# Optimization experiments

Measured on AMD Instinct MI355X. Metric: run time of the kernel, lower is better.

Reference implementation:

```python
import jax, jax.numpy as jnp
import numpy as np

DIM = 1024
HID = 2816
N_ROUTED = 7  # num_experts - num_shared_experts
TOPK = 2
B, S = 4, 2048


def _expert(x, wg, wu, wd):
    # DeepSeekExpertLayer: down(silu(gate(x)) * up(x)); weights stored [in, out]
    return (jax.nn.silu(x @ wg) * (x @ wu)) @ wd


def setup_inputs() -> dict:
    key = jax.random.key(0)
    ks = jax.random.split(key, 9)
    s = 0.02
    x = jax.random.normal(ks[0], (B, S, DIM), jnp.float32)
    shared_gate = jax.random.normal(ks[1], (DIM, HID), jnp.float32) * s
    shared_up = jax.random.normal(ks[2], (DIM, HID), jnp.float32) * s
    shared_down = jax.random.normal(ks[3], (HID, DIM), jnp.float32) * s
    routed_gate = jax.random.normal(ks[4], (N_ROUTED, DIM, HID), jnp.float32) * s
    routed_up = jax.random.normal(ks[5], (N_ROUTED, DIM, HID), jnp.float32) * s
    routed_down = jax.random.normal(ks[6], (N_ROUTED, HID, DIM), jnp.float32) * s
    Wr = jax.random.normal(ks[7], (DIM, N_ROUTED), jnp.float32) * s
    # NOTE: original inits routing_bias to zeros (degenerate routing since logits
    # are MULTIPLIED by it); use random values so routing is non-trivial.
    routing_bias = jax.random.normal(ks[8], (N_ROUTED,), jnp.float32)
    return dict(x=x, shared_gate=shared_gate, shared_up=shared_up, shared_down=shared_down,
                routed_gate=routed_gate, routed_up=routed_up, routed_down=routed_down,
                Wr=Wr, routing_bias=routing_bias)


def reference(x, shared_gate, shared_up, shared_down,
              routed_gate, routed_up, routed_down, Wr, routing_bias):
    b, s, d = x.shape
    n_exp = routed_gate.shape[0]
    # shared expert path (num_shared_experts == 1, no division)
    shared_out = _expert(x, shared_gate, shared_up, shared_down)
    # router: note logits are MULTIPLIED by routing_bias (faithful to source)
    logits = (x @ Wr) * routing_bias            # [b, s, E]
    probs = jax.nn.sigmoid(logits)
    scores, idx = jax.lax.top_k(probs, TOPK)    # [b, s, k]
    scores = scores / scores.sum(-1, keepdims=True)
    # per-token per-expert combine weight via scatter-add of top-k scores
    t = b * s
    xf = x.reshape(t, d)
    weights = jnp.zeros((t, n_exp), x.dtype).at[
        jnp.arange(t)[:, None], idx.reshape(t, TOPK)].add(scores.reshape(t, TOPK))
    combined = jnp.zeros_like(xf)
    for e in range(n_exp):  # static small loop over experts
        combined = combined + _expert(xf, routed_gate[e], routed_up[e], routed_down[e]) * weights[:, e:e + 1]
    return shared_out + combined.reshape(b, s, d)
```

## Files before the change

### kernel.cpp

```cpp
#include <hip/hip_runtime.h>
#include <hip/hip_bf16.h>

#define DIM 1024
#define HID 2816
#define NEXP 7
#define TOKENS 8192

#define MW2_XB    0ull
#define MW2_WGU   16777216ull
#define MW2_WD    109051904ull
#define MW2_H     155189248ull
#define MW2_TOK   298647552ull
#define MW2_WGT   298749440ull
#define MW2_SLT   298851328ull
#define MW2_META  298916864ull
#define MW2_NEED  298918912ull

#define MW_XB    0ull
#define MW_H     16777216ull
#define MW_WGU   114098176ull
#define MW_WD    206372864ull
#define MW_TOK   252510208ull
#define MW_WGT   252579328ull
#define MW_META  252648448ull
#define MW_NEED  252650496ull

typedef __bf16 bf16x8 __attribute__((ext_vector_type(8)));
typedef float f32x4 __attribute__((ext_vector_type(4)));

static __device__ __forceinline__ unsigned short f2b(float f) {
  union { float f; unsigned int i; } c; c.f = f;
  unsigned int i = c.i;
  unsigned int r = (i + 0x7fffu + ((i >> 16) & 1u)) >> 16;
  return (unsigned short)r;
}

static __device__ __forceinline__ void gload16(const void* g, void* l) {
  __builtin_amdgcn_global_load_lds(
      (const __attribute__((address_space(1))) unsigned int*)g,
      (__attribute__((address_space(3))) unsigned int*)l, 16, 0, 0);
}

__global__ __launch_bounds__(256, 2) void router_kernel(
    const float* __restrict__ X,
    const float* __restrict__ Wr,
    const float* __restrict__ bias,
    int* __restrict__ eidx,
    float* __restrict__ ew)
{
  __shared__ float wr[DIM * NEXP];
  for (int i = threadIdx.x; i < DIM * NEXP; i += 256) wr[i] = Wr[i];
  __syncthreads();
  int t = blockIdx.x * 256 + threadIdx.x;
  float acc[NEXP];
#pragma unroll
  for (int e = 0; e < NEXP; ++e) acc[e] = 0.f;
  const float* xp = X + (size_t)t * DIM;
  for (int d0 = 0; d0 < DIM; d0 += 4) {
    float4 xv = *(const float4*)(xp + d0);
    const float* xs = (const float*)&xv;
#pragma unroll
    for (int j = 0; j < 4; ++j) {
      float xf = xs[j];
#pragma unroll
      for (int e = 0; e < NEXP; ++e) acc[e] += xf * wr[(d0 + j) * NEXP + e];
    }
  }
  float p[NEXP];
#pragma unroll
  for (int e = 0; e < NEXP; ++e)
    p[e] = 1.f / (1.f + __expf(-acc[e] * bias[e]));
  float best = -1.f; int bi = 0;
#pragma unroll
  for (int e = 0; e < NEXP; ++e) if (p[e] > best) { best = p[e]; bi = e; }
  float sec = -1.f; int si = 0;
#pragma unroll
  for (int e = 0; e < NEXP; ++e) if (e != bi && p[e] > sec) { sec = p[e]; si = e; }
  float s = best + sec;
  eidx[t] = bi | (si << 8);
  ((float2*)ew)[t] = make_float2(best / s, sec / s);
}

__global__ __launch_bounds__(256) void xcvt_kernel(
    const float* __restrict__ X, unsigned short* __restrict__ Xb)
{
  int i = (blockIdx.x * 256 + threadIdx.x) * 8;
  float4 v0 = *(const float4*)&X[i];
  float4 v1 = *(const float4*)&X[i + 4];
  unsigned short o[8];
  o[0] = f2b(v0.x); o[1] = f2b(v0.y); o[2] = f2b(v0.z); o[3] = f2b(v0.w);
  o[4] = f2b(v1.x); o[5] = f2b(v1.y); o[6] = f2b(v1.z); o[7] = f2b(v1.w);
  *(int4*)&Xb[i] = *(const int4*)o;
}

__global__ __launch_bounds__(256) void build2_kernel(
    const int* __restrict__ eidx, const float* __restrict__ ew,
    int* __restrict__ tok, float* __restrict__ wgt,
    int2* __restrict__ slt, int* __restrict__ meta)
{
  __shared__ int cnt[NEXP], fill[NEXP], ofs[NEXP];
  const int tid = threadIdx.x;
  const int lane = tid & 63, wid = tid >> 6;
  if (tid < NEXP) { cnt[tid] = 0; fill[tid] = 0; }
  for (int i = tid; i < TOKENS; i += 256) { tok[i] = i; wgt[i] = 1.f; }
  __syncthreads();
  const unsigned long long lmask = (1ull << lane) - 1ull;
  for (int base = wid * 64; base < TOKENS; base += 256) {
    int t = base + lane;
    int p = eidx[t];
    int e0 = p & 0xff, e1 = (p >> 8) & 0xff;
#pragma unroll
    for (int e = 0; e < NEXP; ++e) {
      unsigned long long m0 = __ballot(e0 == e);
      unsigned long long m1 = __ballot(e1 == e);
      if (lane == 0) {
        int tot = __popcll(m0) + __popcll(m1);
        if (tot) atomicAdd(&cnt[e], tot);
      }
    }
  }
  __syncthreads();
  if (tid == 0) {
    int o = 0, nb = 0;
    meta[0] = TOKENS; meta[8] = 0;
    for (int i = 0; i < TOKENS / 128; ++i) meta[17 + nb++] = 0 | (i << 4);
    for (int e = 0; e < NEXP; ++e) {
      ofs[e] = o;
      meta[1 + e] = cnt[e];
      meta[9 + e] = TOKENS + o;
      int b = (cnt[e] + 127) >> 7;
      for (int i = 0; i < b; ++i) meta[17 + nb++] = (e + 1) | (i << 4);
      o += b << 7;
    }
    meta[16] = nb;
  }
  __syncthreads();
  for (int base = wid * 64; base < TOKENS; base += 256) {
    int t = base + lane;
    int p = eidx[t];
    int e0 = p & 0xff, e1 = (p >> 8) & 0xff;
    float2 w = ((const float2*)ew)[t];
    int s0 = 0, s1 = 0;
#pragma unroll
    for (int e = 0; e < NEXP; ++e) {
      unsigned long long m0 = __ballot(e0 == e);
      unsigned long long m1 = __ballot(e1 == e);
      int tot = __popcll(m0) + __popcll(m1);
      int wb = 0;
      if (lane == 0 && tot) wb = atomicAdd(&fill[e], tot);
      wb = __shfl(wb, 0);
      if (e0 == e) {
        int sl = TOKENS + ofs[e] + wb + __popcll(m0 & lmask);
        tok[sl] = t; wgt[sl] = w.x; s0 = sl;
      }
      if (e1 == e) {
        int sl = TOKENS + ofs[e] + wb + __popcll(m0) + __popcll(m1 & lmask);
        tok[sl] = t; wgt[sl] = w.y; s1 = sl;
      }
    }
    slt[t] = make_int2(s0, s1);
  }
}

__global__ __launch_bounds__(256) void transpose_all_kernel(
    const float* __restrict__ sg, const float* __restrict__ su, const float* __restrict__ sd,
    const float* __restrict__ rg, const float* __restrict__ ru, const float* __restrict__ rd,
    unsigned short* __restrict__ WguA, unsigned short* __restrict__ WdA)
{
  int b = blockIdx.x;
  int e = b / 2112, r = b % 2112;
  int m = r / 704, q2 = r % 704;
  const float* src; unsigned short* dst; int K, N, nb, kb;
  if (m == 0) {
    src = e ? rg + (size_t)(e - 1) * DIM * HID : sg;
    dst = WguA + (size_t)e * (2 * (size_t)HID * DIM);
    K = DIM; N = HID; nb = q2 % 44; kb = q2 / 44;
  } else if (m == 1) {
    src = e ? ru + (size_t)(e - 1) * DIM * HID : su;
    dst = WguA + (size_t)e * (2 * (size_t)HID * DIM) + (size_t)HID * DIM;
    K = DIM; N = HID; nb = q2 % 44; kb = q2 / 44;
  } else {
    src = e ? rd + (size_t)(e - 1) * HID * DIM : sd;
    dst = WdA + (size_t)e * ((size_t)HID * DIM);
    K = HID; N = DIM; nb = q2 % 16; kb = q2 / 16;
  }
  __shared__ unsigned short t[64][72];
  const int n0 = nb * 64, k0 = kb * 64;
  const int tid = threadIdx.x;
  const int kl = tid >> 4, nl = (tid & 15) * 4;
#pragma unroll
  for (int i = 0; i < 4; ++i) {
    int k = kl + i * 16;
    float4 v = *(const float4*)&src[(size_t)(k0 + k) * N + n0 + nl];
    t[nl + 0][k] = f2b(v.x); t[nl + 1][k] = f2b(v.y);
    t[nl + 2][k] = f2b(v.z); t[nl + 3][k] = f2b(v.w);
  }
  __syncthreads();
  const int nl2 = tid >> 3, kc = (tid & 7) * 8;
#pragma unroll
  for (int i = 0; i < 2; ++i) {
    int n = nl2 + i * 32;
    *(int4*)&dst[(size_t)(n0 + n) * K + k0 + kc] = *(const int4*)&t[n][kc];
  }
}


__global__ __launch_bounds__(256, 2) void gateup_all_kernel(
    const unsigned short* __restrict__ Xb,
    const unsigned short* __restrict__ WguA,
    const int* __restrict__ tok, const float* __restrict__ wgt,
    const int* __restrict__ meta,
    unsigned short* __restrict__ H)
{
  const int yb = blockIdx.y;
  if (yb >= meta[16]) return;
  const int ent = meta[17 + yb];
  const int e = ent & 15, mb = ent >> 4;
  const int cnt = meta[e];
  const int pofs = meta[8 + e];
  const unsigned short* Wg = WguA + (size_t)e * (2 * (size_t)HID * DIM);
  const unsigned short* Wu = Wg + (size_t)HID * DIM;

  __shared__ __align__(16) unsigned short As[128 * 64];
  __shared__ __align__(16) unsigned short Bgs[64 * 64];
  __shared__ __align__(16) unsigned short Bus[64 * 64];
  __shared__ float wl[128];

  const int n0 = blockIdx.x * 64;
  const int tid = threadIdx.x;
  const int lane = tid & 63;
  const int w = tid >> 6;
  const int wm = (w & 1) * 64;
  const int wn = (w >> 1) * 32;
  const int c = lane & 15;
  const int q = lane >> 4;
  const int cx = c & 7;

  if (tid < 128)
    wl[tid] = (mb * 128 + tid < cnt) ? wgt[pofs + mb * 128 + tid] : 0.f;

  const int r8 = lane >> 3;
  const int swz = ((lane & 7) ^ r8) * 8;
  const int wrow = w * 8 + r8;

  const unsigned short* aptr[4];
#pragma unroll
  for (int i = 0; i < 4; ++i) {
    int s = mb * 128 + i * 32 + wrow;
    int t = (s < cnt) ? tok[pofs + s] : 0;
    aptr[i] = Xb + (size_t)t * DIM + swz;
  }
  const unsigned short* gptr[2];
  const unsigned short* uptr[2];
#pragma unroll
  for (int i = 0; i < 2; ++i) {
    gptr[i] = Wg + (size_t)(n0 + i * 32 + wrow) * DIM + swz;
    uptr[i] = Wu + (size_t)(n0 + i * 32 + wrow) * DIM + swz;
  }

  f32x4 accg[4][2], accu[4][2];
#pragma unroll
  for (int mi = 0; mi < 4; ++mi)
#pragma unroll
    for (int ni = 0; ni < 2; ++ni) {
      accg[mi][ni] = {0.f, 0.f, 0.f, 0.f};
      accu[mi][ni] = {0.f, 0.f, 0.f, 0.f};
    }

  for (int k0 = 0; k0 < DIM; k0 += 64) {
    __syncthreads();
#pragma unroll
    for (int i = 0; i < 4; ++i) gload16(aptr[i] + k0, &As[i * 2048 + tid * 8]);
#pragma unroll
    for (int i = 0; i < 2; ++i) {
      gload16(gptr[i] + k0, &Bgs[i * 2048 + tid * 8]);
      gload16(uptr[i] + k0, &Bus[i * 2048 + tid * 8]);
    }
    __syncthreads();
#pragma unroll
    for (int h = 0; h < 2; ++h) {
      const int go = ((h * 4 + q) ^ cx) * 8;
      bf16x8 a[4], bg[2], bu[2];
#pragma unroll
      for (int mi = 0; mi < 4; ++mi)
        a[mi] = *(const bf16x8*)&As[(wm + mi * 16 + c) * 64 + go];
#pragma unroll
      for (int ni = 0; ni < 2; ++ni) {
        bg[ni] = *(const bf16x8*)&Bgs[(wn + ni * 16 + c) * 64 + go];
        bu[ni] = *(const bf16x8*)&Bus[(wn + ni * 16 + c) * 64 + go];
      }
#pragma unroll
      for (int mi = 0; mi < 4; ++mi)
#pragma unroll
        for (int ni = 0; ni < 2; ++ni) {
          accg[mi][ni] = __builtin_amdgcn_mfma_f32_16x16x32_bf16(a[mi], bg[ni], accg[mi][ni], 0, 0, 0);
          accu[mi][ni] = __builtin_amdgcn_mfma_f32_16x16x32_bf16(a[mi], bu[ni], accu[mi][ni], 0, 0, 0);
        }
    }
  }
#pragma unroll
  for (int mi = 0; mi < 4; ++mi)
#pragma unroll
    for (int ni = 0; ni < 2; ++ni)
#pragma unroll
      for (int r = 0; r < 4; ++r) {
        int row = wm + mi * 16 + q * 4 + r;
        int col = wn + ni * 16 + c;
        float g = accg[mi][ni][r];
        float u = accu[mi][ni][r];
        float h = (g / (1.f + __expf(-g))) * u * wl[row];
        H[(size_t)(pofs + mb * 128 + row) * HID + n0 + col] = f2b(h);
      }
}

__global__ __launch_bounds__(256, 2) void down_all_kernel(
    const unsigned short* __restrict__ Hm,
    const unsigned short* __restrict__ WdA,
    const int* __restrict__ meta,
    float* __restrict__ P)
{
  const int yb = blockIdx.y;
  if (yb >= meta[16]) return;
  const int ent = meta[17 + yb];
  const int e = ent & 15, mb = ent >> 4;
  const int pofs = meta[8 + e];
  const unsigned short* WdT = WdA + (size_t)e * ((size_t)HID * DIM);

  __shared__ __align__(16) unsigned short As[128 * 64];
  __shared__ __align__(16) unsigned short Bs[128 * 64];
  const int n0 = blockIdx.x * 128;
  const int tid = threadIdx.x;
  const int lane = tid & 63;
  const int w4 = tid >> 6;
  const int wm = (w4 & 1) * 64;
  const int wn = (w4 >> 1) * 64;
  const int c = lane & 15;
  const int q = lane >> 4;
  const int cx = c & 7;

  const int r8 = lane >> 3;
  const int swz = ((lane & 7) ^ r8) * 8;
  const int wrow = w4 * 8 + r8;

  const unsigned short* aptr[4];
  const unsigned short* bptr[4];
#pragma unroll
  for (int i = 0; i < 4; ++i) {
    aptr[i] = Hm + (size_t)(pofs + mb * 128 + i * 32 + wrow) * HID + swz;
    bptr[i] = WdT + (size_t)(n0 + i * 32 + wrow) * HID + swz;
  }

  f32x4 acc[4][4];
#pragma unroll
  for (int mi = 0; mi < 4; ++mi)
#pragma unroll
    for (int ni = 0; ni < 4; ++ni) acc[mi][ni] = {0.f, 0.f, 0.f, 0.f};

  for (int k0 = 0; k0 < HID; k0 += 64) {
    __syncthreads();
#pragma unroll
    for (int i = 0; i < 4; ++i) {
      gload16(aptr[i] + k0, &As[i * 2048 + tid * 8]);
      gload16(bptr[i] + k0, &Bs[i * 2048 + tid * 8]);
    }
    __syncthreads();
#pragma unroll
    for (int h = 0; h < 2; ++h) {
      const int go = ((h * 4 + q) ^ cx) * 8;
      bf16x8 a[4], b[4];
#pragma unroll
      for (int mi = 0; mi < 4; ++mi)
        a[mi] = *(const bf16x8*)&As[(wm + mi * 16 + c) * 64 + go];
#pragma unroll
      for (int ni = 0; ni < 4; ++ni)
        b[ni] = *(const bf16x8*)&Bs[(wn + ni * 16 + c) * 64 + go];
#pragma unroll
      for (int mi = 0; mi < 4; ++mi)
#pragma unroll
        for (int ni = 0; ni < 4; ++ni)
          acc[mi][ni] = __builtin_amdgcn_mfma_f32_16x16x32_bf16(a[mi], b[ni], acc[mi][ni], 0, 0, 0);
    }
  }
#pragma unroll
  for (int mi = 0; mi < 4; ++mi)
#pragma unroll
    for (int r = 0; r < 4; ++r) {
      int prow = pofs + mb * 128 + wm + mi * 16 + q * 4 + r;
#pragma unroll
      for (int ni = 0; ni < 4; ++ni) {
        int col = n0 + wn + ni * 16 + c;
        P[(size_t)prow * DIM + col] = acc[mi][ni][r];
      }
    }
}

__global__ __launch_bounds__(256) void combine_kernel(
    const float* __restrict__ P, const int2* __restrict__ slt,
    float* __restrict__ out)
{
  const int t = blockIdx.x;
  const int2 s = slt[t];
  const int d = threadIdx.x;
  float4 a = ((const float4*)(P + (size_t)t * DIM))[d];
  float4 b = ((const float4*)(P + (size_t)s.x * DIM))[d];
  float4 cc = ((const float4*)(P + (size_t)s.y * DIM))[d];
  float4 o;
  o.x = a.x + b.x + cc.x; o.y = a.y + b.y + cc.y;
  o.z = a.z + b.z + cc.z; o.w = a.w + b.w + cc.w;
  ((float4*)(out + (size_t)t * DIM))[d] = o;
}

__global__ __launch_bounds__(256) void build_kernel(
    const int* __restrict__ eidx, const float* __restrict__ ew,
    int* __restrict__ tok, float* __restrict__ wgt, int* __restrict__ meta,
    int padmode)
{
  __shared__ int cnt[NEXP], fill[NEXP], ofs[NEXP];
  if (threadIdx.x < NEXP) { cnt[threadIdx.x] = 0; fill[threadIdx.x] = 0; }
  __syncthreads();
  for (int t = threadIdx.x; t < TOKENS; t += 256) {
    int p = eidx[t];
    atomicAdd(&cnt[p & 0xff], 1);
    atomicAdd(&cnt[(p >> 8) & 0xff], 1);
  }
  __syncthreads();
  if (threadIdx.x == 0) {
    int o = 0, nb = 0;
    for (int e = 0; e < NEXP; ++e) {
      ofs[e] = o;
      meta[e] = cnt[e];
      meta[8 + e] = o;
      if (padmode) {
        int b = (cnt[e] + 127) >> 7;
        for (int i = 0; i < b; ++i) meta[16 + nb++] = e | (i << 3);
        o += b << 7;
      } else {
        o += cnt[e];
      }
    }
    meta[15] = nb;
  }
  __syncthreads();
  for (int t = threadIdx.x; t < TOKENS; t += 256) {
    int p = eidx[t];
    int e0 = p & 0xff, e1 = (p >> 8) & 0xff;
    float2 w = ((const float2*)ew)[t];
    int p0 = ofs[e0] + atomicAdd(&fill[e0], 1);
    tok[p0] = t; wgt[p0] = w.x;
    int p1 = ofs[e1] + atomicAdd(&fill[e1], 1);
    tok[p1] = t; wgt[p1] = w.y;
  }
}

__global__ __launch_bounds__(256, 2) void gateup_kernel(
    const unsigned short* __restrict__ Xb,
    const unsigned short* __restrict__ Wgu,
    unsigned short* __restrict__ H)
{
  __shared__ __align__(16) unsigned short As[128 * 64];
  __shared__ __align__(16) unsigned short Bgs[64 * 64];
  __shared__ __align__(16) unsigned short Bus[64 * 64];
  const int m0 = blockIdx.y * 128;
  const int n0 = blockIdx.x * 64;
  const int tid = threadIdx.x;
  const int lane = tid & 63;
  const int w = tid >> 6;
  const int wm = (w & 1) * 64;
  const int wn = (w >> 1) * 32;
  const int c = lane & 15;
  const int q = lane >> 4;
  const int cx = c & 7;
  const unsigned short* Wg = Wgu;
  const unsigned short* Wu = Wgu + (size_t)HID * DIM;
  const int r8 = lane >> 3;
  const int swz = ((lane & 7) ^ r8) * 8;
  const int wrow = w * 8 + r8;
  const unsigned short* aptr[4];
#pragma unroll
  for (int i = 0; i < 4; ++i)
    aptr[i] = Xb + (size_t)(m0 + i * 32 + wrow) * DIM + swz;
  const unsigned short* gptr[2];
  const unsigned short* uptr[2];
#pragma unroll
  for (int i = 0; i < 2; ++i) {
    gptr[i] = Wg + (size_t)(n0 + i * 32 + wrow) * DIM + swz;
    uptr[i] = Wu + (size_t)(n0 + i * 32 + wrow) * DIM + swz;
  }
  f32x4 accg[4][2], accu[4][2];
#pragma unroll
  for (int mi = 0; mi < 4; ++mi)
#pragma unroll
    for (int ni = 0; ni < 2; ++ni) {
      accg[mi][ni] = {0.f, 0.f, 0.f, 0.f};
      accu[mi][ni] = {0.f, 0.f, 0.f, 0.f};
    }
  for (int k0 = 0; k0 < DIM; k0 += 64) {
    __syncthreads();
#pragma unroll
    for (int i = 0; i < 4; ++i) gload16(aptr[i] + k0, &As[i * 2048 + tid * 8]);
#pragma unroll
    for (int i = 0; i < 2; ++i) {
      gload16(gptr[i] + k0, &Bgs[i * 2048 + tid * 8]);
      gload16(uptr[i] + k0, &Bus[i * 2048 + tid * 8]);
    }
    __syncthreads();
#pragma unroll
    for (int h = 0; h < 2; ++h) {
      const int go = ((h * 4 + q) ^ cx) * 8;
      bf16x8 a[4], bg[2], bu[2];
#pragma unroll
      for (int mi = 0; mi < 4; ++mi)
        a[mi] = *(const bf16x8*)&As[(wm + mi * 16 + c) * 64 + go];
#pragma unroll
      for (int ni = 0; ni < 2; ++ni) {
        bg[ni] = *(const bf16x8*)&Bgs[(wn + ni * 16 + c) * 64 + go];
        bu[ni] = *(const bf16x8*)&Bus[(wn + ni * 16 + c) * 64 + go];
      }
#pragma unroll
      for (int mi = 0; mi < 4; ++mi)
#pragma unroll
        for (int ni = 0; ni < 2; ++ni) {
          accg[mi][ni] = __builtin_amdgcn_mfma_f32_16x16x32_bf16(a[mi], bg[ni], accg[mi][ni], 0, 0, 0);
          accu[mi][ni] = __builtin_amdgcn_mfma_f32_16x16x32_bf16(a[mi], bu[ni], accu[mi][ni], 0, 0, 0);
        }
    }
  }
#pragma unroll
  for (int mi = 0; mi < 4; ++mi)
#pragma unroll
    for (int ni = 0; ni < 2; ++ni)
#pragma unroll
      for (int r = 0; r < 4; ++r) {
        int row = wm + mi * 16 + q * 4 + r;
        int col = wn + ni * 16 + c;
        float g = accg[mi][ni][r];
        float u = accu[mi][ni][r];
        float h = (g / (1.f + __expf(-g))) * u;
        H[(size_t)(m0 + row) * HID + n0 + col] = f2b(h);
      }
}

__global__ __launch_bounds__(256, 2) void gateup_sparse_all_kernel(
    const unsigned short* __restrict__ Xb,
    const unsigned short* __restrict__ WguR,
    const int* __restrict__ tok, const float* __restrict__ wgt,
    const int* __restrict__ meta,
    unsigned short* __restrict__ H)
{
  const int yb = blockIdx.y;
  if (yb >= meta[15]) return;
  const int bm = meta[16 + yb];
  const int e = bm & 7, mb = bm >> 3;
  const int cnt = meta[e];
  const int pofs = meta[8 + e];
  const unsigned short* Wgu = WguR + (size_t)e * (2 * (size_t)HID * DIM);
  __shared__ __align__(16) unsigned short As[128 * 64];
  __shared__ __align__(16) unsigned short Bgs[64 * 64];
  __shared__ __align__(16) unsigned short Bus[64 * 64];
  __shared__ float wl[128];
  const int n0 = blockIdx.x * 64;
  const int tid = threadIdx.x;
  const int lane = tid & 63;
  const int w = tid >> 6;
  const int wm = (w & 1) * 64;
  const int wn = (w >> 1) * 32;
  const int c = lane & 15;
  const int q = lane >> 4;
  const int cx = c & 7;
  if (tid < 128)
    wl[tid] = (mb * 128 + tid < cnt) ? wgt[pofs + mb * 128 + tid] : 0.f;
  const unsigned short* Wg = Wgu;
  const unsigned short* Wu = Wgu + (size_t)HID * DIM;
  const int r8 = lane >> 3;
  const int swz = ((lane & 7) ^ r8) * 8;
  const int wrow = w * 8 + r8;
  const unsigned short* aptr[4];
#pragma unroll
  for (int i = 0; i < 4; ++i) {
    int s = mb * 128 + i * 32 + wrow;
    int t = (s < cnt) ? tok[pofs + s] : 0;
    aptr[i] = Xb + (size_t)t * DIM + swz;
  }
  const unsigned short* gptr[2];
  const unsigned short* uptr[2];
#pragma unroll
  for (int i = 0; i < 2; ++i) {
    gptr[i] = Wg + (size_t)(n0 + i * 32 + wrow) * DIM + swz;
    uptr[i] = Wu + (size_t)(n0 + i * 32 + wrow) * DIM + swz;
  }
  f32x4 accg[4][2], accu[4][2];
#pragma unroll
  for (int mi = 0; mi < 4; ++mi)
#pragma unroll
    for (int ni = 0; ni < 2; ++ni) {
      accg[mi][ni] = {0.f, 0.f, 0.f, 0.f};
      accu[mi][ni] = {0.f, 0.f, 0.f, 0.f};
    }
  for (int k0 = 0; k0 < DIM; k0 += 64) {
    __syncthreads();
#pragma unroll
    for (int i = 0; i < 4; ++i) gload16(aptr[i] + k0, &As[i * 2048 + tid * 8]);
#pragma unroll
    for (int i = 0; i < 2; ++i) {
      gload16(gptr[i] + k0, &Bgs[i * 2048 + tid * 8]);
      gload16(uptr[i] + k0, &Bus[i * 2048 + tid * 8]);
    }
    __syncthreads();
#pragma unroll
    for (int h = 0; h < 2; ++h) {
      const int go = ((h * 4 + q) ^ cx) * 8;
      bf16x8 a[4], bg[2], bu[2];
#pragma unroll
      for (int mi = 0; mi < 4; ++mi)
        a[mi] = *(const bf16x8*)&As[(wm + mi * 16 + c) * 64 + go];
#pragma unroll
      for (int ni = 0; ni < 2; ++ni) {
        bg[ni] = *(const bf16x8*)&Bgs[(wn + ni * 16 + c) * 64 + go];
        bu[ni] = *(const bf16x8*)&Bus[(wn + ni * 16 + c) * 64 + go];
      }
#pragma unroll
      for (int mi = 0; mi < 4; ++mi)
#pragma unroll
        for (int ni = 0; ni < 2; ++ni) {
          accg[mi][ni] = __builtin_amdgcn_mfma_f32_16x16x32_bf16(a[mi], bg[ni], accg[mi][ni], 0, 0, 0);
          accu[mi][ni] = __builtin_amdgcn_mfma_f32_16x16x32_bf16(a[mi], bu[ni], accu[mi][ni], 0, 0, 0);
        }
    }
  }
#pragma unroll
  for (int mi = 0; mi < 4; ++mi)
#pragma unroll
    for (int ni = 0; ni < 2; ++ni)
#pragma unroll
      for (int r = 0; r < 4; ++r) {
        int row = wm + mi * 16 + q * 4 + r;
        int col = wn + ni * 16 + c;
        float g = accg[mi][ni][r];
        float u = accu[mi][ni][r];
        float h = (g / (1.f + __expf(-g))) * u * wl[row];
        H[(size_t)(pofs + mb * 128 + row) * HID + n0 + col] = f2b(h);
      }
}

__global__ __launch_bounds__(256, 2) void down_dense_kernel(
    const unsigned short* __restrict__ Hm,
    const unsigned short* __restrict__ WdT,
    float* __restrict__ out)
{
  __shared__ __align__(16) unsigned short As[128 * 64];
  __shared__ __align__(16) unsigned short Bs[128 * 64];
  const int m0 = blockIdx.y * 128;
  const int n0 = blockIdx.x * 128;
  const int tid = threadIdx.x;
  const int lane = tid & 63;
  const int w4 = tid >> 6;
  const int wm = (w4 & 1) * 64;
  const int wn = (w4 >> 1) * 64;
  const int c = lane & 15;
  const int q = lane >> 4;
  const int cx = c & 7;
  const int r8 = lane >> 3;
  const int swz = ((lane & 7) ^ r8) * 8;
  const int wrow = w4 * 8 + r8;
  const unsigned short* aptr[4];
  const unsigned short* bptr[4];
#pragma unroll
  for (int i = 0; i < 4; ++i) {
    aptr[i] = Hm + (size_t)(m0 + i * 32 + wrow) * HID + swz;
    bptr[i] = WdT + (size_t)(n0 + i * 32 + wrow) * HID + swz;
  }
  f32x4 acc[4][4];
#pragma unroll
  for (int mi = 0; mi < 4; ++mi)
#pragma unroll
    for (int ni = 0; ni < 4; ++ni) acc[mi][ni] = {0.f, 0.f, 0.f, 0.f};
  for (int k0 = 0; k0 < HID; k0 += 64) {
    __syncthreads();
#pragma unroll
    for (int i = 0; i < 4; ++i) {
      gload16(aptr[i] + k0, &As[i * 2048 + tid * 8]);
      gload16(bptr[i] + k0, &Bs[i * 2048 + tid * 8]);
    }
    __syncthreads();
#pragma unroll
    for (int h = 0; h < 2; ++h) {
      const int go = ((h * 4 + q) ^ cx) * 8;
      bf16x8 a[4], b[4];
#pragma unroll
      for (int mi = 0; mi < 4; ++mi)
        a[mi] = *(const bf16x8*)&As[(wm + mi * 16 + c) * 64 + go];
#pragma unroll
      for (int ni = 0; ni < 4; ++ni)
        b[ni] = *(const bf16x8*)&Bs[(wn + ni * 16 + c) * 64 + go];
#pragma unroll
      for (int mi = 0; mi < 4; ++mi)
#pragma unroll
        for (int ni = 0; ni < 4; ++ni)
          acc[mi][ni] = __builtin_amdgcn_mfma_f32_16x16x32_bf16(a[mi], b[ni], acc[mi][ni], 0, 0, 0);
    }
  }
#pragma unroll
  for (int mi = 0; mi < 4; ++mi)
#pragma unroll
    for (int r = 0; r < 4; ++r) {
      int trow = m0 + wm + mi * 16 + q * 4 + r;
#pragma unroll
      for (int ni = 0; ni < 4; ++ni) {
        int col = n0 + wn + ni * 16 + c;
        out[(size_t)trow * DIM + col] = acc[mi][ni][r];
      }
    }
}

__global__ __launch_bounds__(256, 2) void down_sparse_all_kernel(
    const unsigned short* __restrict__ Hm,
    const unsigned short* __restrict__ WdR,
    const int* __restrict__ tok, const int* __restrict__ meta,
    float* __restrict__ out)
{
  const int yb = blockIdx.y;
  if (yb >= meta[15]) return;
  const int bm = meta[16 + yb];
  const int e = bm & 7, mb = bm >> 3;
  const int cnt = meta[e];
  const int pofs = meta[8 + e];
  const unsigned short* WdT = WdR + (size_t)e * ((size_t)HID * DIM);
  const int kbase = blockIdx.z * (HID / 2);
  __shared__ __align__(16) unsigned short As[128 * 64];
  __shared__ __align__(16) unsigned short Bs[128 * 64];
  __shared__ int tl[128];
  const int n0 = blockIdx.x * 128;
  const int tid = threadIdx.x;
  const int lane = tid & 63;
  const int w4 = tid >> 6;
  const int wm = (w4 & 1) * 64;
  const int wn = (w4 >> 1) * 64;
  const int c = lane & 15;
  const int q = lane >> 4;
  const int cx = c & 7;
  if (tid < 128)
    tl[tid] = (mb * 128 + tid < cnt) ? tok[pofs + mb * 128 + tid] : 0;
  const int r8 = lane >> 3;
  const int swz = ((lane & 7) ^ r8) * 8;
  const int wrow = w4 * 8 + r8;
  const unsigned short* aptr[4];
  const unsigned short* bptr[4];
#pragma unroll
  for (int i = 0; i < 4; ++i) {
    aptr[i] = Hm + (size_t)(pofs + mb * 128 + i * 32 + wrow) * HID + kbase + swz;
    bptr[i] = WdT + (size_t)(n0 + i * 32 + wrow) * HID + kbase + swz;
  }
  f32x4 acc[4][4];
#pragma unroll
  for (int mi = 0; mi < 4; ++mi)
#pragma unroll
    for (int ni = 0; ni < 4; ++ni) acc[mi][ni] = {0.f, 0.f, 0.f, 0.f};
  for (int k0 = 0; k0 < HID / 2; k0 += 64) {
    __syncthreads();
#pragma unroll
    for (int i = 0; i < 4; ++i) {
      gload16(aptr[i] + k0, &As[i * 2048 + tid * 8]);
      gload16(bptr[i] + k0, &Bs[i * 2048 + tid * 8]);
    }
    __syncthreads();
#pragma unroll
    for (int h = 0; h < 2; ++h) {
      const int go = ((h * 4 + q) ^ cx) * 8;
      bf16x8 a[4], b[4];
#pragma unroll
      for (int mi = 0; mi < 4; ++mi)
        a[mi] = *(const bf16x8*)&As[(wm + mi * 16 + c) * 64 + go];
#pragma unroll
      for (int ni = 0; ni < 4; ++ni)
        b[ni] = *(const bf16x8*)&Bs[(wn + ni * 16 + c) * 64 + go];
#pragma unroll
      for (int mi = 0; mi < 4; ++mi)
#pragma unroll
        for (int ni = 0; ni < 4; ++ni)
          acc[mi][ni] = __builtin_amdgcn_mfma_f32_16x16x32_bf16(a[mi], b[ni], acc[mi][ni], 0, 0, 0);
    }
  }
#pragma unroll
  for (int mi = 0; mi < 4; ++mi)
#pragma unroll
    for (int r = 0; r < 4; ++r) {
      int lr = wm + mi * 16 + q * 4 + r;
      if (mb * 128 + lr < cnt) {
        int t = tl[lr];
#pragma unroll
        for (int ni = 0; ni < 4; ++ni) {
          int col = n0 + wn + ni * 16 + c;
          atomicAdd(&out[(size_t)t * DIM + col], acc[mi][ni][r]);
        }
      }
    }
}

extern "C" void kernel_launch(void* const* d_in, const int* in_sizes, int n_in,
                              void* d_out, int out_size, void* d_ws, size_t ws_size,
                              hipStream_t stream) {
  (void)in_sizes; (void)n_in; (void)out_size;
  const float* x   = (const float*)d_in[0];
  const float* sg  = (const float*)d_in[1];
  const float* su  = (const float*)d_in[2];
  const float* sd  = (const float*)d_in[3];
  const float* rg  = (const float*)d_in[4];
  const float* ru  = (const float*)d_in[5];
  const float* rd  = (const float*)d_in[6];
  const float* wrr = (const float*)d_in[7];
  const float* rb  = (const float*)d_in[8];
  float* out = (float*)d_out;

  char* ws = (char*)d_ws;
  dim3 blk(256);

  if (ws_size >= MW2_NEED) {
    unsigned short* Xb   = (unsigned short*)(ws + MW2_XB);
    unsigned short* WguA = (unsigned short*)(ws + MW2_WGU);
    unsigned short* WdA  = (unsigned short*)(ws + MW2_WD);
    unsigned short* H    = (unsigned short*)(ws + MW2_H);
    int*   tok           = (int*)(ws + MW2_TOK);
    float* wgt           = (float*)(ws + MW2_WGT);
    int2*  slt           = (int2*)(ws + MW2_SLT);
    int*   meta          = (int*)(ws + MW2_META);
    float* P             = (float*)ws;
    int*   eidx = (int*)H;
    float* ew   = (float*)((char*)H + 32768);

    router_kernel<<<dim3(TOKENS / 256), blk, 0, stream>>>(x, wrr, rb, eidx, ew);
    xcvt_kernel<<<dim3(TOKENS * DIM / (8 * 256)), blk, 0, stream>>>(x, Xb);
    build2_kernel<<<dim3(1), blk, 0, stream>>>(eidx, ew, tok, wgt, slt, meta);
    transpose_all_kernel<<<dim3(8 * 2112), blk, 0, stream>>>(sg, su, sd, rg, ru, rd, WguA, WdA);
    gateup_all_kernel<<<dim3(HID / 64, 199), blk, 0, stream>>>(Xb, WguA, tok, wgt, meta, H);
    down_all_kernel<<<dim3(DIM / 128, 199), blk, 0, stream>>>(H, WdA, meta, P);
    combine_kernel<<<dim3(TOKENS), blk, 0, stream>>>(P, slt, out);
  } else {
    unsigned short* Xb   = (unsigned short*)(ws + MW_XB);
    unsigned short* H    = (unsigned short*)(ws + MW_H);
    unsigned short* WguA = (unsigned short*)(ws + MW_WGU);
    unsigned short* WdA  = (unsigned short*)(ws + MW_WD);
    int*   tok           = (int*)(ws + MW_TOK);
    float* wgt           = (float*)(ws + MW_WGT);
    int*   meta          = (int*)(ws + MW_META);
    int*   eidx = (int*)H;
    float* ew   = (float*)((char*)H + 32768);

    router_kernel<<<dim3(TOKENS / 256), blk, 0, stream>>>(x, wrr, rb, eidx, ew);
    xcvt_kernel<<<dim3(TOKENS * DIM / (8 * 256)), blk, 0, stream>>>(x, Xb);
    build_kernel<<<dim3(1), blk, 0, stream>>>(eidx, ew, tok, wgt, meta, 1);
    transpose_all_kernel<<<dim3(8 * 2112), blk, 0, stream>>>(sg, su, sd, rg, ru, rd, WguA, WdA);
    gateup_kernel<<<dim3(HID / 64, TOKENS / 128), blk, 0, stream>>>(Xb, WguA, H);
    down_dense_kernel<<<dim3(DIM / 128, TOKENS / 128), blk, 0, stream>>>(H, WdA, out);
    const unsigned short* WguRt = WguA + 2 * (size_t)HID * DIM;
    const unsigned short* WdRt  = WdA + (size_t)HID * DIM;
    gateup_sparse_all_kernel<<<dim3(HID / 64, 135), blk, 0, stream>>>(Xb, WguRt, tok, wgt, meta, H);
    down_sparse_all_kernel<<<dim3(DIM / 128, 135, 2), blk, 0, stream>>>(H, WdRt, tok, meta, out);
  }
}
```

Before: 972.8 us.

## Rewrite grouped gate/up GEMM as 512-thread 256-row tile with triple-buffered pipeline

Replaces the gate/up expert GEMM with a 512-thread kernel that handles 256-token tiles, triple-buffers the A and B operand tiles in shared memory, and interleaves async global loads with MFMA phases. It uses explicit barriers, waitcnt, sched_barrier and setprio to overlap memory with compute. Routing metadata is rebuilt with 256-row padding for gateup and a separate 128-row block list for the down kernel, and the workspace layout grows accordingly. The goal is to hide load latency and improve reuse of the weight tiles. The cost is more padding waste per expert, a large shared-memory footprint that limits occupancy, and hand-written wait counts that must be exactly right for correctness.

```diff
diff --git a/kernel.cpp b/kernel.cpp
--- a/kernel.cpp
+++ b/kernel.cpp
@@ -5,16 +5,17 @@
 #define HID 2816
 #define NEXP 7
 #define TOKENS 8192
-
-#define MW2_XB    0ull
-#define MW2_WGU   16777216ull
-#define MW2_WD    109051904ull
-#define MW2_H     155189248ull
-#define MW2_TOK   298647552ull
-#define MW2_WGT   298749440ull
-#define MW2_SLT   298851328ull
-#define MW2_META  298916864ull
-#define MW2_NEED  298918912ull
+#define NT16 (DIM / 64)
+
+#define MW3_XB    0ull
+#define MW3_WGU   16777216ull
+#define MW3_WD    109051904ull
+#define MW3_H     155189248ull
+#define MW3_TOK   303693824ull
+#define MW3_WGT   303799296ull
+#define MW3_SLT   303904768ull
+#define MW3_META  303970304ull
+#define MW3_NEED  303972352ull
 
 #define MW_XB    0ull
 #define MW_H     16777216ull
@@ -93,7 +94,7 @@
   *(int4*)&Xb[i] = *(const int4*)o;
 }
 
-__global__ __launch_bounds__(256) void build2_kernel(
+__global__ __launch_bounds__(256) void build3_kernel(
     const int* __restrict__ eidx, const float* __restrict__ ew,
     int* __restrict__ tok, float* __restrict__ wgt,
     int2* __restrict__ slt, int* __restrict__ meta)
@@ -121,18 +122,20 @@
   }
   __syncthreads();
   if (tid == 0) {
-    int o = 0, nb = 0;
+    int o = 0, nb = 0, nb2 = 0;
     meta[0] = TOKENS; meta[8] = 0;
-    for (int i = 0; i < TOKENS / 128; ++i) meta[17 + nb++] = 0 | (i << 4);
+    for (int i = 0; i < TOKENS / 256; ++i) meta[32 + nb++] = 0 | (i << 4);
+    for (int i = 0; i < TOKENS / 128; ++i) meta[160 + nb2++] = 0 | (i << 4);
     for (int e = 0; e < NEXP; ++e) {
       ofs[e] = o;
       meta[1 + e] = cnt[e];
       meta[9 + e] = TOKENS + o;
-      int b = (cnt[e] + 127) >> 7;
-      for (int i = 0; i < b; ++i) meta[17 + nb++] = (e + 1) | (i << 4);
-      o += b << 7;
-    }
-    meta[16] = nb;
+      int b = (cnt[e] + 255) >> 8;
+      for (int i = 0; i < b; ++i)     meta[32 + nb++]   = (e + 1) | (i << 4);
+      for (int i = 0; i < 2 * b; ++i) meta[160 + nb2++] = (e + 1) | (i << 4);
+      o += b << 8;
+    }
+    meta[16] = nb; meta[17] = nb2;
   }
   __syncthreads();
   for (int base = wid * 64; base < TOKENS; base += 256) {
@@ -204,8 +207,7 @@
   }
 }
 
-
-__global__ __launch_bounds__(256, 2) void gateup_all_kernel(
+__global__ __launch_bounds__(512, 2) void gateup8_kernel(
     const unsigned short* __restrict__ Xb,
     const unsigned short* __restrict__ WguA,
     const int* __restrict__ tok, const float* __restrict__ wgt,
@@ -214,49 +216,52 @@
 {
   const int yb = blockIdx.y;
   if (yb >= meta[16]) return;
-  const int ent = meta[17 + yb];
+  const int ent = meta[32 + yb];
   const int e = ent & 15, mb = ent >> 4;
   const int cnt = meta[e];
   const int pofs = meta[8 + e];
+  const int m0 = mb * 256;
   const unsigned short* Wg = WguA + (size_t)e * (2 * (size_t)HID * DIM);
   const unsigned short* Wu = Wg + (size_t)HID * DIM;
 
-  __shared__ __align__(16) unsigned short As[128 * 64];
-  __shared__ __align__(16) unsigned short Bgs[64 * 64];
-  __shared__ __align__(16) unsigned short Bus[64 * 64];
-  __shared__ float wl[128];
-
-  const int n0 = blockIdx.x * 64;
+  __shared__ __align__(16) unsigned short As[3][256 * 64];
+  __shared__ __align__(16) unsigned short Bgs[3][64 * 64];
+  __shared__ __align__(16) unsigned short Bus[3][64 * 64];
+  __shared__ float wl[256];
+
   const int tid = threadIdx.x;
   const int lane = tid & 63;
   const int w = tid >> 6;
-  const int wm = (w & 1) * 64;
-  const int wn = (w >> 1) * 32;
+  const int wmi = w & 3;
+  const int wni = w >> 2;
   const int c = lane & 15;
   const int q = lane >> 4;
   const int cx = c & 7;
 
-  if (tid < 128)
-    wl[tid] = (mb * 128 + tid < cnt) ? wgt[pofs + mb * 128 + tid] : 0.f;
-
-  const int r8 = lane >> 3;
-  const int swz = ((lane & 7) ^ r8) * 8;
-  const int wrow = w * 8 + r8;
+  const int srow = tid >> 3;
+  const int swz = ((tid & 7) ^ (srow & 7)) * 8;
 
   const unsigned short* aptr[4];
 #pragma unroll
   for (int i = 0; i < 4; ++i) {
-    int s = mb * 128 + i * 32 + wrow;
+    int s = m0 + i * 64 + srow;
     int t = (s < cnt) ? tok[pofs + s] : 0;
     aptr[i] = Xb + (size_t)t * DIM + swz;
   }
-  const unsigned short* gptr[2];
-  const unsigned short* uptr[2];
-#pragma unroll
-  for (int i = 0; i < 2; ++i) {
-    gptr[i] = Wg + (size_t)(n0 + i * 32 + wrow) * DIM + swz;
-    uptr[i] = Wu + (size_t)(n0 + i * 32 + wrow) * DIM + swz;
-  }
+  const int n0 = blockIdx.x * 64;
+  const unsigned short* gptr = Wg + (size_t)(n0 + srow) * DIM + swz;
+  const unsigned short* uptr = Wu + (size_t)(n0 + srow) * DIM + swz;
+
+  if (tid < 256) wl[tid] = (m0 + tid < cnt) ? wgt[pofs + m0 + tid] : 0.f;
+
+#pragma unroll
+  for (int t = 0; t < 2; ++t) {
+#pragma unroll
+    for (int i = 0; i < 4; ++i) gload16(aptr[i] + t * 64, &As[t][i * 4096 + tid * 8]);
+    gload16(gptr + t * 64, &Bgs[t][tid * 8]);
+    gload16(uptr + t * 64, &Bus[t][tid * 8]);
+  }
+  __syncthreads();
 
   f32x4 accg[4][2], accu[4][2];
 #pragma unroll
@@ -267,49 +272,89 @@
       accu[mi][ni] = {0.f, 0.f, 0.f, 0.f};
     }
 
-  for (int k0 = 0; k0 < DIM; k0 += 64) {
-    __syncthreads();
-#pragma unroll
-    for (int i = 0; i < 4; ++i) gload16(aptr[i] + k0, &As[i * 2048 + tid * 8]);
-#pragma unroll
-    for (int i = 0; i < 2; ++i) {
-      gload16(gptr[i] + k0, &Bgs[i * 2048 + tid * 8]);
-      gload16(uptr[i] + k0, &Bus[i * 2048 + tid * 8]);
-    }
-    __syncthreads();
-#pragma unroll
-    for (int h = 0; h < 2; ++h) {
-      const int go = ((h * 4 + q) ^ cx) * 8;
-      bf16x8 a[4], bg[2], bu[2];
-#pragma unroll
-      for (int mi = 0; mi < 4; ++mi)
-        a[mi] = *(const bf16x8*)&As[(wm + mi * 16 + c) * 64 + go];
+  int b = 0, bs = 2;
+#pragma unroll 1
+  for (int t = 0; t < NT16; ++t) {
+    bf16x8 a[4][2], bg[2][2];
+#pragma unroll
+    for (int mi = 0; mi < 4; ++mi)
+#pragma unroll
+      for (int ks = 0; ks < 2; ++ks)
+        a[mi][ks] = *(const bf16x8*)&As[b][(wmi * 64 + mi * 16 + c) * 64 + (((ks * 4 + q) ^ cx) * 8)];
+#pragma unroll
+    for (int ni = 0; ni < 2; ++ni)
+#pragma unroll
+      for (int ks = 0; ks < 2; ++ks)
+        bg[ni][ks] = *(const bf16x8*)&Bgs[b][(wni * 32 + ni * 16 + c) * 64 + (((ks * 4 + q) ^ cx) * 8)];
+    if (t + 2 < NT16) {
+      const int k2 = (t + 2) * 64;
+      gload16(aptr[0] + k2, &As[bs][0 * 4096 + tid * 8]);
+      gload16(aptr[1] + k2, &As[bs][1 * 4096 + tid * 8]);
+      gload16(aptr[2] + k2, &As[bs][2 * 4096 + tid * 8]);
+    }
+    __builtin_amdgcn_s_barrier();
+    asm volatile("s_waitcnt lgkmcnt(0)" ::: "memory");
+    __builtin_amdgcn_sched_barrier(0);
+    __builtin_amdgcn_s_setprio(1);
+#pragma unroll
+    for (int mi = 0; mi < 4; ++mi)
 #pragma unroll
       for (int ni = 0; ni < 2; ++ni) {
-        bg[ni] = *(const bf16x8*)&Bgs[(wn + ni * 16 + c) * 64 + go];
-        bu[ni] = *(const bf16x8*)&Bus[(wn + ni * 16 + c) * 64 + go];
-      }
-#pragma unroll
-      for (int mi = 0; mi < 4; ++mi)
-#pragma unroll
-        for (int ni = 0; ni < 2; ++ni) {
-          accg[mi][ni] = __builtin_amdgcn_mfma_f32_16x16x32_bf16(a[mi], bg[ni], accg[mi][ni], 0, 0, 0);
-          accu[mi][ni] = __builtin_amdgcn_mfma_f32_16x16x32_bf16(a[mi], bu[ni], accu[mi][ni], 0, 0, 0);
-        }
-    }
-  }
-#pragma unroll
-  for (int mi = 0; mi < 4; ++mi)
+        accg[mi][ni] = __builtin_amdgcn_mfma_f32_16x16x32_bf16(a[mi][0], bg[ni][0], accg[mi][ni], 0, 0, 0);
+        accg[mi][ni] = __builtin_amdgcn_mfma_f32_16x16x32_bf16(a[mi][1], bg[ni][1], accg[mi][ni], 0, 0, 0);
+      }
+    __builtin_amdgcn_s_setprio(0);
+    __builtin_amdgcn_sched_barrier(0);
+    __builtin_amdgcn_s_barrier();
+    __builtin_amdgcn_sched_barrier(0);
+
+    bf16x8 bu[2][2];
 #pragma unroll
     for (int ni = 0; ni < 2; ++ni)
 #pragma unroll
+      for (int ks = 0; ks < 2; ++ks)
+        bu[ni][ks] = *(const bf16x8*)&Bus[b][(wni * 32 + ni * 16 + c) * 64 + (((ks * 4 + q) ^ cx) * 8)];
+    if (t + 2 < NT16) {
+      const int k2 = (t + 2) * 64;
+      gload16(aptr[3] + k2, &As[bs][3 * 4096 + tid * 8]);
+      gload16(gptr + k2, &Bgs[bs][tid * 8]);
+      gload16(uptr + k2, &Bus[bs][tid * 8]);
+      asm volatile("s_waitcnt vmcnt(6)" ::: "memory");
+    } else if (t + 1 < NT16) {
+      asm volatile("s_waitcnt vmcnt(0)" ::: "memory");
+    }
+    __builtin_amdgcn_s_barrier();
+    asm volatile("s_waitcnt lgkmcnt(0)" ::: "memory");
+    __builtin_amdgcn_sched_barrier(0);
+    __builtin_amdgcn_s_setprio(1);
+#pragma unroll
+    for (int mi = 0; mi < 4; ++mi)
+#pragma unroll
+      for (int ni = 0; ni < 2; ++ni) {
+        accu[mi][ni] = __builtin_amdgcn_mfma_f32_16x16x32_bf16(a[mi][0], bu[ni][0], accu[mi][ni], 0, 0, 0);
+        accu[mi][ni] = __builtin_amdgcn_mfma_f32_16x16x32_bf16(a[mi][1], bu[ni][1], accu[mi][ni], 0, 0, 0);
+      }
+    __builtin_amdgcn_s_setprio(0);
+    __builtin_amdgcn_sched_barrier(0);
+    __builtin_amdgcn_s_barrier();
+    __builtin_amdgcn_sched_barrier(0);
+
+    b = (b == 2) ? 0 : b + 1;
+    bs = (bs == 2) ? 0 : bs + 1;
+  }
+
+#pragma unroll
+  for (int mi = 0; mi < 4; ++mi)
+#pragma unroll
+    for (int ni = 0; ni < 2; ++ni)
+#pragma unroll
       for (int r = 0; r < 4; ++r) {
-        int row = wm + mi * 16 + q * 4 + r;
-        int col = wn + ni * 16 + c;
+        int row = wmi * 64 + mi * 16 + q * 4 + r;
+        int col = wni * 32 + ni * 16 + c;
         float g = accg[mi][ni][r];
         float u = accu[mi][ni][r];
         float h = (g / (1.f + __expf(-g))) * u * wl[row];
-        H[(size_t)(pofs + mb * 128 + row) * HID + n0 + col] = f2b(h);
+        H[(size_t)(pofs + m0 + row) * HID + n0 + col] = f2b(h);
       }
 }
 
@@ -320,8 +365,8 @@
     float* __restrict__ P)
 {
   const int yb = blockIdx.y;
-  if (yb >= meta[16]) return;
-  const int ent = meta[17 + yb];
+  if (yb >= meta[17]) return;
+  const int ent = meta[160 + yb];
   const int e = ent & 15, mb = ent >> 4;
   const int pofs = meta[8 + e];
   const unsigned short* WdT = WdA + (size_t)e * ((size_t)HID * DIM);
@@ -367,18 +412,18 @@
 #pragma unroll
     for (int h = 0; h < 2; ++h) {
       const int go = ((h * 4 + q) ^ cx) * 8;
-      bf16x8 a[4], b[4];
+      bf16x8 a[4], bb[4];
 #pragma unroll
       for (int mi = 0; mi < 4; ++mi)
         a[mi] = *(const bf16x8*)&As[(wm + mi * 16 + c) * 64 + go];
 #pragma unroll
       for (int ni = 0; ni < 4; ++ni)
-        b[ni] = *(const bf16x8*)&Bs[(wn + ni * 16 + c) * 64 + go];
+        bb[ni] = *(const bf16x8*)&Bs[(wn + ni * 16 + c) * 64 + go];
 #pragma unroll
       for (int mi = 0; mi < 4; ++mi)
 #pragma unroll
         for (int ni = 0; ni < 4; ++ni)
-          acc[mi][ni] = __builtin_amdgcn_mfma_f32_16x16x32_bf16(a[mi], b[ni], acc[mi][ni], 0, 0, 0);
+          acc[mi][ni] = __builtin_amdgcn_mfma_f32_16x16x32_bf16(a[mi], bb[ni], acc[mi][ni], 0, 0, 0);
     }
   }
 #pragma unroll
@@ -685,18 +730,18 @@
 #pragma unroll
     for (int h = 0; h < 2; ++h) {
       const int go = ((h * 4 + q) ^ cx) * 8;
-      bf16x8 a[4], b[4];
+      bf16x8 a[4], bb[4];
 #pragma unroll
       for (int mi = 0; mi < 4; ++mi)
         a[mi] = *(const bf16x8*)&As[(wm + mi * 16 + c) * 64 + go];
 #pragma unroll
       for (int ni = 0; ni < 4; ++ni)
-        b[ni] = *(const bf16x8*)&Bs[(wn + ni * 16 + c) * 64 + go];
+        bb[ni] = *(const bf16x8*)&Bs[(wn + ni * 16 + c) * 64 + go];
 #pragma unroll
       for (int mi = 0; mi < 4; ++mi)
 #pragma unroll
         for (int ni = 0; ni < 4; ++ni)
-          acc[mi][ni] = __builtin_amdgcn_mfma_f32_16x16x32_bf16(a[mi], b[ni], acc[mi][ni], 0, 0, 0);
+          acc[mi][ni] = __builtin_amdgcn_mfma_f32_16x16x32_bf16(a[mi], bb[ni], acc[mi][ni], 0, 0, 0);
     }
   }
 #pragma unroll
@@ -747,7 +792,7 @@
   const unsigned short* bptr[4];
 #pragma unroll
   for (int i = 0; i < 4; ++i) {
-    aptr[i] = Hm + (size_t)(pofs + mb * 128 + i * 32 + wrow) * HID + kbase + swz;
+    aptr[i] = Hm + (size_t)(mb * 128 + i * 32 + wrow) * HID + kbase + swz;
     bptr[i] = WdT + (size_t)(n0 + i * 32 + wrow) * HID + kbase + swz;
   }
   f32x4 acc[4][4];
@@ -766,18 +811,18 @@
 #pragma unroll
     for (int h = 0; h < 2; ++h) {
       const int go = ((h * 4 + q) ^ cx) * 8;
-      bf16x8 a[4], b[4];
+      bf16x8 a[4], bb[4];
 #pragma unroll
       for (int mi = 0; mi < 4; ++mi)
         a[mi] = *(const bf16x8*)&As[(wm + mi * 16 + c) * 64 + go];
 #pragma unroll
       for (int ni = 0; ni < 4; ++ni)
-        b[ni] = *(const bf16x8*)&Bs[(wn + ni * 16 + c) * 64 + go];
+        bb[ni] = *(const bf16x8*)&Bs[(wn + ni * 16 + c) * 64 + go];
 #pragma unroll
       for (int mi = 0; mi < 4; ++mi)
 #pragma unroll
         for (int ni = 0; ni < 4; ++ni)
-          acc[mi][ni] = __builtin_amdgcn_mfma_f32_16x16x32_bf16(a[mi], b[ni], acc[mi][ni], 0, 0, 0);
+          acc[mi][ni] = __builtin_amdgcn_mfma_f32_16x16x32_bf16(a[mi], bb[ni], acc[mi][ni], 0, 0, 0);
     }
   }
 #pragma unroll
@@ -814,25 +859,25 @@
   char* ws = (char*)d_ws;
   dim3 blk(256);
 
-  if (ws_size >= MW2_NEED) {
-    unsigned short* Xb   = (unsigned short*)(ws + MW2_XB);
-    unsigned short* WguA = (unsigned short*)(ws + MW2_WGU);
-    unsigned short* WdA  = (unsigned short*)(ws + MW2_WD);
-    unsigned short* H    = (unsigned short*)(ws + MW2_H);
-    int*   tok           = (int*)(ws + MW2_TOK);
-    float* wgt           = (float*)(ws + MW2_WGT);
-    int2*  slt           = (int2*)(ws + MW2_SLT);
-    int*   meta          = (int*)(ws + MW2_META);
+  if (ws_size >= MW3_NEED) {
+    unsigned short* Xb   = (unsigned short*)(ws + MW3_XB);
+    unsigned short* WguA = (unsigned short*)(ws + MW3_WGU);
+    unsigned short* WdA  = (unsigned short*)(ws + MW3_WD);
+    unsigned short* H    = (unsigned short*)(ws + MW3_H);
+    int*   tok           = (int*)(ws + MW3_TOK);
+    float* wgt           = (float*)(ws + MW3_WGT);
+    int2*  slt           = (int2*)(ws + MW3_SLT);
+    int*   meta          = (int*)(ws + MW3_META);
     float* P             = (float*)ws;
     int*   eidx = (int*)H;
     float* ew   = (float*)((char*)H + 32768);
 
     router_kernel<<<dim3(TOKENS / 256), blk, 0, stream>>>(x, wrr, rb, eidx, ew);
     xcvt_kernel<<<dim3(TOKENS * DIM / (8 * 256)), blk, 0, stream>>>(x, Xb);
-    build2_kernel<<<dim3(1), blk, 0, stream>>>(eidx, ew, tok, wgt, slt, meta);
+    build3_kernel<<<dim3(1), blk, 0, stream>>>(eidx, ew, tok, wgt, slt, meta);
     transpose_all_kernel<<<dim3(8 * 2112), blk, 0, stream>>>(sg, su, sd, rg, ru, rd, WguA, WdA);
-    gateup_all_kernel<<<dim3(HID / 64, 199), blk, 0, stream>>>(Xb, WguA, tok, wgt, meta, H);
-    down_all_kernel<<<dim3(DIM / 128, 199), blk, 0, stream>>>(H, WdA, meta, P);
+    gateup8_kernel<<<dim3(HID / 64, 104), dim3(512), 0, stream>>>(Xb, WguA, tok, wgt, meta, H);
+    down_all_kernel<<<dim3(DIM / 128, 208), blk, 0, stream>>>(H, WdA, meta, P);
     combine_kernel<<<dim3(TOKENS), blk, 0, stream>>>(P, slt, out);
   } else {
     unsigned short* Xb   = (unsigned short*)(ws + MW_XB);
```

Measured after the change: 1.036 ms. 6.5% more time.
